# Optimization experiments

Hardware: AMD Instinct MI355X
Metric: run time of the kernel (lower is better)

Reference implementation:

```python
import jax, jax.numpy as jnp
from jax import lax
import numpy as np

B, CTX, TGT, D_MODEL = 2, 1024, 256, 512
EXPAND, D_STATE, D_CONV, N_LAYERS = 2, 16, 4, 2
D_INNER = EXPAND * D_MODEL
DT_RANK = (D_MODEL + 15) // 16  # 32, mamba_ssm default ceil(d_model/16)
LN_EPS = 1e-5


def setup_inputs() -> dict:
    key = jax.random.key(0)
    ks = jax.random.split(key, 20)
    s = 0.02
    inp = {
        "context_repr": jax.random.normal(ks[0], (B, CTX, D_MODEL), jnp.float32),
        "target_time_emb": jax.random.normal(ks[1], (B, TGT, D_MODEL), jnp.float32),
        "target_var_emb": jax.random.normal(ks[2], (B, TGT, D_MODEL), jnp.float32),
        "target_count": TGT,
        # position_proj / output_proj / LayerNorm params
        "pos_w": jax.random.normal(ks[3], (D_MODEL, 2 * D_MODEL), jnp.float32) * s,
        "pos_b": jnp.zeros((D_MODEL,), jnp.float32),
        "outp_w": jax.random.normal(ks[4], (D_MODEL, D_MODEL), jnp.float32) * s,
        "outp_b": jnp.zeros((D_MODEL,), jnp.float32),
        "ln_g": jnp.ones((D_MODEL,), jnp.float32),
        "ln_b": jnp.zeros((D_MODEL,), jnp.float32),
        # stacked per-layer Mamba params
        "in_w": jax.random.normal(ks[5], (N_LAYERS, 2 * D_INNER, D_MODEL), jnp.float32) * s,
        "conv_w": jax.random.normal(ks[6], (N_LAYERS, D_INNER, D_CONV), jnp.float32) * s,
        "conv_b": jnp.zeros((N_LAYERS, D_INNER), jnp.float32),
        "xproj_w": jax.random.normal(ks[7], (N_LAYERS, DT_RANK + 2 * D_STATE, D_INNER), jnp.float32) * s,
        "dt_w": jax.random.normal(ks[8], (N_LAYERS, D_INNER, DT_RANK), jnp.float32) * s,
        "dt_b": jax.random.normal(ks[9], (N_LAYERS, D_INNER), jnp.float32) * s,
        # A_log init as in mamba_ssm: A = arange(1, d_state+1) repeated over d_inner
        "A_log": jnp.broadcast_to(
            jnp.log(jnp.arange(1, D_STATE + 1, dtype=jnp.float32)),
            (N_LAYERS, D_INNER, D_STATE),
        ).copy(),
        "D_skip": jnp.ones((N_LAYERS, D_INNER), jnp.float32),
        "out_w": jax.random.normal(ks[10], (N_LAYERS, D_MODEL, D_INNER), jnp.float32) * s,
    }
    return inp


def _mamba_block(x, in_w, conv_w, conv_b, xproj_w, dt_w, dt_b, A_log, D_skip, out_w):
    # x: [B, L, d_model]
    Bb, L, _ = x.shape
    xz = jnp.einsum("bld,ed->ble", x, in_w)          # [B, L, 2*d_inner]
    xc, z = jnp.split(xz, 2, axis=-1)
    # causal depthwise conv1d (Conv1d pad=d_conv-1 then [..., :L])
    xt = xc.transpose(0, 2, 1)                        # [B, d_inner, L]
    conv = lax.conv_general_dilated(
        xt, conv_w[:, None, :], (1,), [(D_CONV - 1, 0)],
        feature_group_count=D_INNER,
        dimension_numbers=("NCH", "OIH", "NCH"),
    )
    u = jax.nn.silu(conv + conv_b[None, :, None]).transpose(0, 2, 1)  # [B, L, d_inner]
    x_dbl = jnp.einsum("bld,ed->ble", u, xproj_w)     # [B, L, dt_rank + 2*d_state]
    dt, Bm, Cm = jnp.split(x_dbl, [DT_RANK, DT_RANK + D_STATE], axis=-1)
    delta = jax.nn.softplus(jnp.einsum("blr,dr->bld", dt, dt_w) + dt_b)  # [B, L, d_inner]
    A = -jnp.exp(A_log)                               # [d_inner, d_state]
    dA = jnp.exp(delta[..., None] * A)                # [B, L, d_inner, d_state]
    dBu = delta[..., None] * Bm[:, :, None, :] * u[..., None]

    def step(h, inps):
        dA_t, dBu_t, C_t = inps                       # [B,d_inner,d_state], same, [B,d_state]
        h = dA_t * h + dBu_t
        y = jnp.einsum("bds,bs->bd", h, C_t)
        return h, y

    h0 = jnp.zeros((Bb, D_INNER, D_STATE), x.dtype)
    _, ys = lax.scan(step, h0, (dA.transpose(1, 0, 2, 3), dBu.transpose(1, 0, 2, 3), Cm.transpose(1, 0, 2)))
    y = ys.transpose(1, 0, 2) + u * D_skip            # [B, L, d_inner]
    y = y * jax.nn.silu(z)
    return jnp.einsum("ble,de->bld", y, out_w)        # [B, L, d_model]


def reference(context_repr, target_time_emb, target_var_emb, target_count,
              pos_w, pos_b, outp_w, outp_b, ln_g, ln_b,
              in_w, conv_w, conv_b, xproj_w, dt_w, dt_b, A_log, D_skip, out_w):
    tc = jnp.concatenate([target_time_emb, target_var_emb], axis=-1)      # [B, T, 2*d]
    pos = jnp.einsum("blk,dk->bld", tc, pos_w) + pos_b                    # [B, T, d]
    x = jnp.concatenate([context_repr, pos], axis=1)                      # [B, C+T, d]
    for i in range(N_LAYERS):
        x = x + _mamba_block(x, in_w[i], conv_w[i], conv_b[i], xproj_w[i],
                             dt_w[i], dt_b[i], A_log[i], D_skip[i], out_w[i])
    mu = jnp.mean(x, axis=-1, keepdims=True)
    var = jnp.mean(jnp.square(x - mu), axis=-1, keepdims=True)
    x = (x - mu) * lax.rsqrt(var + LN_EPS) * ln_g + ln_b
    tgt = x[:, -int(target_count):]
    return jnp.einsum("bld,ed->ble", tgt, outp_w) + outp_b
```

## Files before the change

### kernel.cpp

```cpp
#include <hip/hip_runtime.h>
#include <hip/hip_bf16.h>

#define B_     2
#define CTX_   1024
#define TGT_   256
#define DM_    512
#define L_     1280
#define DI_    1024
#define DS_    16
#define DCONV_ 4
#define NL_    2
#define DTR_   32
#define MROWS_ (B_*L_)
#define NC_    80
#define CL_    16
#define XDBL_N_ (MROWS_*64)

typedef unsigned short u16;
typedef __attribute__((ext_vector_type(8))) __bf16 bf16x8;
typedef __attribute__((ext_vector_type(4))) float f32x4;

__device__ __forceinline__ float sigmoidf_(float v){ return 1.f/(1.f+__expf(-v)); }
__device__ __forceinline__ float siluf_(float v){ return v*sigmoidf_(v); }
__device__ __forceinline__ float softplusf_(float v){ return (v>20.f)?v:log1pf(__expf(v)); }
__device__ __forceinline__ u16 f2b(float f){
    union { float f; unsigned u; } x; x.f = f;
    unsigned u = x.u;
    return (u16)((u + 0x7fffu + ((u>>16)&1u)) >> 16);
}
__device__ __forceinline__ float b2f(u16 v){ return __uint_as_float(((unsigned)v)<<16); }
__device__ __forceinline__ void gload_lds16(const void* g, void* l){
    __builtin_amdgcn_global_load_lds((const __attribute__((address_space(1))) unsigned*)g,
                                     (__attribute__((address_space(3))) unsigned*)l, 16, 0, 0);
}

#define G0_ 262144
#define G1_ 131072
#define G2_  65536
#define G3_  32768
#define G4_  16384
__global__ __launch_bounds__(256) void k_f2b_all(const float* __restrict__ s0, const float* __restrict__ s1,
                                                 const float* __restrict__ s2, const float* __restrict__ s3,
                                                 const float* __restrict__ s4,
                                                 u16* d0, u16* d1, u16* d2, u16* d3, u16* d4){
    int g = blockIdx.x*256 + threadIdx.x;
    const float* s; u16* d; int base;
    if      (g < G0_)                { s=s0; d=d0; base=g*8; }
    else if (g < G0_+G1_)            { s=s1; d=d1; base=(g-G0_)*8; }
    else if (g < G0_+G1_+G2_)        { s=s2; d=d2; base=(g-G0_-G1_)*8; }
    else if (g < G0_+G1_+G2_+G3_)    { s=s3; d=d3; base=(g-G0_-G1_-G2_)*8; }
    else                             { s=s4; d=d4; base=(g-G0_-G1_-G2_-G3_)*8; }
    float4 a = *(const float4*)&s[base];
    float4 b = *(const float4*)&s[base+4];
    union { u16 us[8]; uint4 v; } o;
    o.us[0]=f2b(a.x); o.us[1]=f2b(a.y); o.us[2]=f2b(a.z); o.us[3]=f2b(a.w);
    o.us[4]=f2b(b.x); o.us[5]=f2b(b.y); o.us[6]=f2b(b.z); o.us[7]=f2b(b.w);
    *(uint4*)&d[base] = o.v;
}

__global__ __launch_bounds__(256) void k_pre(const float* __restrict__ ctx, const float* __restrict__ te,
                                             const float* __restrict__ ve, float* __restrict__ x,
                                             u16* __restrict__ xb, u16* __restrict__ tcb){
    int blk = blockIdx.x;
    if (blk < 1024){
        int e = (blk*256 + threadIdx.x)*4;
        int d = e % DM_;
        int l = (e/DM_) % CTX_;
        int b = e/(DM_*CTX_);
        float4 v = *(const float4*)&ctx[e];
        size_t o = ((size_t)(b*L_+l))*DM_ + d;
        *(float4*)&x[o] = v;
        union { u16 us[4]; uint2 q; } p;
        p.us[0]=f2b(v.x); p.us[1]=f2b(v.y); p.us[2]=f2b(v.z); p.us[3]=f2b(v.w);
        *(uint2*)&xb[o] = p.q;
    } else {
        int e = ((blk-1024)*256 + threadIdx.x)*4;
        int k = e % (2*DM_);
        int r = e / (2*DM_);
        float4 v = (k < DM_) ? *(const float4*)&te[(size_t)r*DM_ + k]
                             : *(const float4*)&ve[(size_t)r*DM_ + (k-DM_)];
        union { u16 us[4]; uint2 q; } p;
        p.us[0]=f2b(v.x); p.us[1]=f2b(v.y); p.us[2]=f2b(v.z); p.us[3]=f2b(v.w);
        *(uint2*)&tcb[e] = p.q;
    }
}

__global__ __launch_bounds__(256) void k_conv_silu(const u16* __restrict__ xzb, const float* __restrict__ cw,
                                                   const float* __restrict__ cb, u16* __restrict__ ub){
    int e = (blockIdx.x*256 + threadIdx.x)*4;
    int d = e % DI_;
    int l = (e/DI_) % L_;
    int b = e/(DI_*L_);
    const u16* base = xzb + (size_t)b*L_*2048 + d;
    float4 w0 = *(const float4*)&cw[(d+0)*4];
    float4 w1 = *(const float4*)&cw[(d+1)*4];
    float4 w2 = *(const float4*)&cw[(d+2)*4];
    float4 w3 = *(const float4*)&cw[(d+3)*4];
    float4 bb = *(const float4*)&cb[d];
    float a0=bb.x, a1=bb.y, a2=bb.z, a3=bb.w;
    #pragma unroll
    for (int k=0;k<DCONV_;++k){
        int ll = l-3+k;
        if (ll >= 0){
            uint2 q = *(const uint2*)&base[(size_t)ll*2048];
            float x0=b2f((u16)(q.x&0xffffu)), x1=b2f((u16)(q.x>>16));
            float x2=b2f((u16)(q.y&0xffffu)), x3=b2f((u16)(q.y>>16));
            float c0 = (k==0)?w0.x:(k==1)?w0.y:(k==2)?w0.z:w0.w;
            float c1 = (k==0)?w1.x:(k==1)?w1.y:(k==2)?w1.z:w1.w;
            float c2 = (k==0)?w2.x:(k==1)?w2.y:(k==2)?w2.z:w2.w;
            float c3 = (k==0)?w3.x:(k==1)?w3.y:(k==2)?w3.z:w3.w;
            a0=fmaf(x0,c0,a0); a1=fmaf(x1,c1,a1); a2=fmaf(x2,c2,a2); a3=fmaf(x3,c3,a3);
        }
    }
    union { u16 us[4]; uint2 q; } o;
    o.us[0]=f2b(siluf_(a0)); o.us[1]=f2b(siluf_(a1));
    o.us[2]=f2b(siluf_(a2)); o.us[3]=f2b(siluf_(a3));
    *(uint2*)&ub[e] = o.q;
}

template<bool WB>
__global__ __launch_bounds__(256) void k_mmx(const u16* __restrict__ A, int lda,
                                             const u16* __restrict__ Bw, int ldb,
                                             float* __restrict__ C, int ldc,
                                             const float* __restrict__ bias, int K,
                                             u16* __restrict__ Cb, int ldcb){
    __shared__ u16 As[128*32];
    __shared__ u16 Bs[128*32];
    int tid = threadIdx.x;
    int wave = tid >> 6, lane = tid & 63;
    int bm = blockIdx.y*128, bn = blockIdx.x*128;
    int wr = (wave>>1)*64, wc = (wave&1)*64;
    f32x4 acc[4][4] = {};
    int lrow = lane & 15, lk = (lane>>4)*8;
    int dphys0 = wave*1024 + lane*16;
    int dphys1 = dphys0 + 4096;
    int alog0  = dphys0 ^ (((dphys0>>7)&7)<<4);
    int alog1  = dphys1 ^ (((dphys1>>7)&7)<<4);
    int grow0  = alog0 >> 6,        grow1  = alog1 >> 6;
    int gcol0  = (alog0 & 63) >> 1, gcol1  = (alog1 & 63) >> 1;
    u16* AsW0 = &As[wave*512];         u16* AsW1 = &As[2048 + wave*512];
    u16* BsW0 = &Bs[wave*512];         u16* BsW1 = &Bs[2048 + wave*512];
    int aoff[4], boff[4];
    #pragma unroll
    for (int f=0; f<4; ++f){
        int ra = wr + f*16 + lrow, rb = wc + f*16 + lrow;
        aoff[f] = (ra*64 + lk*2) ^ (((ra>>1)&7)<<4);
        boff[f] = (rb*64 + lk*2) ^ (((rb>>1)&7)<<4);
    }
    for (int k0 = 0; k0 < K; k0 += 32){
        gload_lds16(&A [(size_t)(bm+grow0)*lda + k0 + gcol0], AsW0);
        gload_lds16(&A [(size_t)(bm+grow1)*lda + k0 + gcol1], AsW1);
        gload_lds16(&Bw[(size_t)(bn+grow0)*ldb + k0 + gcol0], BsW0);
        gload_lds16(&Bw[(size_t)(bn+grow1)*ldb + k0 + gcol1], BsW1);
        __syncthreads();
        bf16x8 af[4], bfr[4];
        #pragma unroll
        for (int f=0; f<4; ++f){
            af [f] = *(const bf16x8*)((const char*)As + aoff[f]);
            bfr[f] = *(const bf16x8*)((const char*)Bs + boff[f]);
        }
        #pragma unroll
        for (int fm=0; fm<4; ++fm)
            #pragma unroll
            for (int fn=0; fn<4; ++fn)
                acc[fm][fn] = __builtin_amdgcn_mfma_f32_16x16x32_bf16(af[fm], bfr[fn], acc[fm][fn], 0,0,0);
        __syncthreads();
    }
    #pragma unroll
    for (int fm=0; fm<4; ++fm){
        int m0 = bm + wr + fm*16 + (lane>>4)*4;
        #pragma unroll
        for (int fn=0; fn<4; ++fn){
            int n = bn + wc + fn*16 + (lane&15);
            float bsv = (!WB && bias) ? bias[n] : 0.f;
            #pragma unroll
            for (int j=0; j<4; ++j){
                float v = acc[fm][fn][j] + bsv;
                if (WB) Cb[(size_t)(m0+j)*ldcb + n] = f2b(v);
                else    C [(size_t)(m0+j)*ldc  + n] = v;
            }
        }
    }
}

template<bool ACC, bool SPLIT, bool SCAT>
__global__ __launch_bounds__(256) void k_mmx64(const u16* __restrict__ A, int lda,
                                               const u16* __restrict__ Bw, int ldb,
                                               float* __restrict__ C, int ldc,
                                               const float* __restrict__ bias, int ksteps,
                                               u16* __restrict__ Cb, int ldcb, int splitStride){
    __shared__ u16 As[64*32];
    __shared__ u16 Bs[64*32];
    int tid = threadIdx.x;
    int wave = tid >> 6, lane = tid & 63;
    int bm = blockIdx.y*64;
    int bn    = SPLIT ? 0 : blockIdx.x*64;
    int kbase = SPLIT ? blockIdx.x*ksteps*32 : 0;
    int wr = (wave>>1)*32, wc = (wave&1)*32;
    f32x4 acc[2][2] = {};
    int lrow = lane & 15, lk = (lane>>4)*8;
    int dphys = wave*1024 + lane*16;
    int alog  = dphys ^ (((dphys>>7)&7)<<4);
    int grow  = alog >> 6;
    int gcol  = (alog & 63) >> 1;
    u16* AsW = &As[wave*512];
    u16* BsW = &Bs[wave*512];
    int aoff[2], boff[2];
    #pragma unroll
    for (int f=0; f<2; ++f){
        int ra = wr + f*16 + lrow, rb = wc + f*16 + lrow;
        aoff[f] = (ra*64 + lk*2) ^ (((ra>>1)&7)<<4);
        boff[f] = (rb*64 + lk*2) ^ (((rb>>1)&7)<<4);
    }
    for (int s = 0; s < ksteps; ++s){
        int k0 = kbase + s*32;
        gload_lds16(&A [(size_t)(bm+grow)*lda + k0 + gcol], AsW);
        gload_lds16(&Bw[(size_t)(bn+grow)*ldb + k0 + gcol], BsW);
        __syncthreads();
        bf16x8 af[2], bfr[2];
        #pragma unroll
        for (int f=0; f<2; ++f){
            af [f] = *(const bf16x8*)((const char*)As + aoff[f]);
            bfr[f] = *(const bf16x8*)((const char*)Bs + boff[f]);
        }
        #pragma unroll
        for (int fm=0; fm<2; ++fm)
            #pragma unroll
            for (int fn=0; fn<2; ++fn)
                acc[fm][fn] = __builtin_amdgcn_mfma_f32_16x16x32_bf16(af[fm], bfr[fn], acc[fm][fn], 0,0,0);
        __syncthreads();
    }
    float* Cout = SPLIT ? (C + (size_t)blockIdx.x*splitStride) : C;
    #pragma unroll
    for (int fm=0; fm<2; ++fm){
        int m0 = bm + wr + fm*16 + (lane>>4)*4;
        #pragma unroll
        for (int fn=0; fn<2; ++fn){
            int n = bn + wc + fn*16 + (lane&15);
            float bsv = (!SPLIT && bias) ? bias[n] : 0.f;
            #pragma unroll
            for (int j=0; j<4; ++j){
                float v = acc[fm][fn][j] + bsv;
                int m = m0 + j;
                if (SCAT){
                    int xrow = (m>>8)*L_ + CTX_ + (m&255);
                    C [(size_t)xrow*ldc  + n] = v;
                    Cb[(size_t)xrow*ldcb + n] = f2b(v);
                } else {
                    size_t off = (size_t)m*ldc + n;
                    if (ACC) v += Cout[off];
                    Cout[off] = v;
                    if (!SPLIT && Cb) Cb[(size_t)m*ldcb + n] = f2b(v);
                }
            }
        }
    }
}

__global__ __launch_bounds__(256) void k_red8(const float* __restrict__ part, float* __restrict__ out){
    int j = (blockIdx.x*256 + threadIdx.x)*4;
    float4 s = *(const float4*)&part[j];
    #pragma unroll
    for (int p=1;p<8;++p){
        float4 t = *(const float4*)&part[(size_t)p*XDBL_N_ + j];
        s.x+=t.x; s.y+=t.y; s.z+=t.z; s.w+=t.w;
    }
    *(float4*)&out[j] = s;
}

__global__ __launch_bounds__(256) void k_scan1(const u16* __restrict__ ub, const float* __restrict__ xdbl,
                                               const float* __restrict__ dtw, const float* __restrict__ dtb,
                                               const float* __restrict__ Alog,
                                               float* __restrict__ hend, float* __restrict__ P){
    __shared__ float sX[CL_*64];
    __shared__ float sW[64*33];
    __shared__ float sDtb[64];
    __shared__ float sDel[CL_*64];
    __shared__ u16   sU[CL_*64];
    int blk = blockIdx.x;
    int dgrp = blk & 15;
    int c = (blk>>4) % NC_;
    int b = blk/(16*NC_);
    int d0 = dgrp*64;
    int tid = threadIdx.x;
    size_t rowbase = (size_t)(b*L_ + c*CL_);
    {
        int e = tid*4;
        *(float4*)&sX[e] = *(const float4*)&xdbl[rowbase*64 + e];
        int st=e>>6, dd=e&63;
        *(uint2*)&sU[e] = *(const uint2*)&ub[(rowbase+st)*DI_ + d0 + dd];
        int w0 = tid*8, dr = w0>>5, kk = w0&31;
        float4 wa = *(const float4*)&dtw[(size_t)(d0+dr)*DTR_ + kk];
        float4 wb = *(const float4*)&dtw[(size_t)(d0+dr)*DTR_ + kk + 4];
        sW[dr*33+kk+0]=wa.x; sW[dr*33+kk+1]=wa.y; sW[dr*33+kk+2]=wa.z; sW[dr*33+kk+3]=wa.w;
        sW[dr*33+kk+4]=wb.x; sW[dr*33+kk+5]=wb.y; sW[dr*33+kk+6]=wb.z; sW[dr*33+kk+7]=wb.w;
        if (tid < 64) sDtb[tid] = dtb[d0+tid];
    }
    __syncthreads();
    #pragma unroll
    for (int i=0;i<4;++i){
        int idx = tid + i*256;
        int t = idx>>6, dd = idx&63;
        float acc = sDtb[dd];
        #pragma unroll
        for (int k=0;k<DTR_;++k) acc = fmaf(sX[t*64+k], sW[dd*33+k], acc);
        sDel[idx] = softplusf_(acc);
    }
    __syncthreads();
    int dl = tid>>2, sg = (tid&3)*4;
    int d = d0 + dl;
    float A[4];
    #pragma unroll
    for (int i=0;i<4;++i) A[i] = -__expf(Alog[d*DS_ + sg + i]);
    float h[4] = {0,0,0,0}, Pl[4] = {1.f,1.f,1.f,1.f};
    #pragma unroll
    for (int t=0;t<CL_;++t){
        float delta = sDel[t*64+dl];
        float uu    = b2f(sU[t*64+dl]);
        float du    = delta*uu;
        #pragma unroll
        for (int i=0;i<4;++i){
            float a = __expf(delta*A[i]);
            h[i]  = fmaf(a, h[i], du*sX[t*64 + 32 + sg + i]);
            Pl[i] *= a;
        }
    }
    size_t ob = ((size_t)((b*NC_+c)*DI_) + d)*DS_ + sg;
    *(float4*)&hend[ob] = make_float4(h[0],h[1],h[2],h[3]);
    *(float4*)&P[ob]    = make_float4(Pl[0],Pl[1],Pl[2],Pl[3]);
}

__global__ __launch_bounds__(256) void k_scan2(float* __restrict__ hend, const float* __restrict__ P){
    int g = blockIdx.x*256 + threadIdx.x;
    int s = g & 15;
    int d = (g>>4) & 1023;
    int b = g>>14;
    size_t base = ((size_t)b*NC_*DI_ + d)*DS_ + s;
    const size_t cs = (size_t)DI_*DS_;
    float h = 0.f;
    for (int c0=0;c0<NC_;c0+=8){
        float he[8], p[8];
        #pragma unroll
        for (int j=0;j<8;++j){ size_t idx = base + (size_t)(c0+j)*cs; he[j]=hend[idx]; p[j]=P[idx]; }
        #pragma unroll
        for (int j=0;j<8;++j){ size_t idx = base + (size_t)(c0+j)*cs; hend[idx]=h; h=fmaf(p[j],h,he[j]); }
    }
}

__global__ __launch_bounds__(256) void k_scan3(const u16* __restrict__ ub, const float* __restrict__ xdbl,
                                               const float* __restrict__ dtw, const float* __restrict__ dtb,
                                               const u16* __restrict__ xzb,
                                               const float* __restrict__ Alog, const float* __restrict__ Dsk,
                                               const float* __restrict__ hstart, u16* __restrict__ yb){
    __shared__ float sX[CL_*64];
    __shared__ float sW[64*33];
    __shared__ float sDtb[64];
    __shared__ float sDel[CL_*64];
    __shared__ u16   sU[CL_*64];
    __shared__ float sY[CL_*64];
    int blk = blockIdx.x;
    int dgrp = blk & 15;
    int c = (blk>>4) % NC_;
    int b = blk/(16*NC_);
    int d0 = dgrp*64;
    int tid = threadIdx.x;
    size_t rowbase = (size_t)(b*L_ + c*CL_);
    {
        int e = tid*4;
        *(float4*)&sX[e] = *(const float4*)&xdbl[rowbase*64 + e];
        int st=e>>6, dd=e&63;
        *(uint2*)&sU[e] = *(const uint2*)&ub[(rowbase+st)*DI_ + d0 + dd];
        int w0 = tid*8, dr = w0>>5, kk = w0&31;
        float4 wa = *(const float4*)&dtw[(size_t)(d0+dr)*DTR_ + kk];
        float4 wb = *(const float4*)&dtw[(size_t)(d0+dr)*DTR_ + kk + 4];
        sW[dr*33+kk+0]=wa.x; sW[dr*33+kk+1]=wa.y; sW[dr*33+kk+2]=wa.z; sW[dr*33+kk+3]=wa.w;
        sW[dr*33+kk+4]=wb.x; sW[dr*33+kk+5]=wb.y; sW[dr*33+kk+6]=wb.z; sW[dr*33+kk+7]=wb.w;
        if (tid < 64) sDtb[tid] = dtb[d0+tid];
    }
    __syncthreads();
    #pragma unroll
    for (int i=0;i<4;++i){
        int idx = tid + i*256;
        int t = idx>>6, dd = idx&63;
        float acc = sDtb[dd];
        #pragma unroll
        for (int k=0;k<DTR_;++k) acc = fmaf(sX[t*64+k], sW[dd*33+k], acc);
        sDel[idx] = softplusf_(acc);
    }
    __syncthreads();
    int dl = tid>>2, sg = (tid&3)*4;
    int d = d0 + dl;
    float A[4];
    #pragma unroll
    for (int i=0;i<4;++i) A[i] = -__expf(Alog[d*DS_ + sg + i]);
    size_t ib = ((size_t)((b*NC_+c)*DI_) + d)*DS_ + sg;
    float4 h4 = *(const float4*)&hstart[ib];
    float h[4] = {h4.x, h4.y, h4.z, h4.w};
    #pragma unroll
    for (int t=0;t<CL_;++t){
        float delta = sDel[t*64+dl];
        float uu    = b2f(sU[t*64+dl]);
        float du    = delta*uu;
        float yt = 0.f;
        #pragma unroll
        for (int i=0;i<4;++i){
            float a = __expf(delta*A[i]);
            h[i] = fmaf(a, h[i], du*sX[t*64 + 32 + sg + i]);
            yt   = fmaf(h[i], sX[t*64 + 48 + sg + i], yt);
        }
        yt += __shfl_xor(yt, 1);
        yt += __shfl_xor(yt, 2);
        if ((tid&3)==0) sY[t*64+dl] = yt;
    }
    __syncthreads();
    {
        int e = tid*4, st = e>>6, dd = e&63;
        size_t off = (rowbase+st)*DI_ + d0 + dd;
        float4 dskv = *(const float4*)&Dsk[d0+dd];
        uint2 zz = *(const uint2*)&xzb[(rowbase+st)*2048 + DI_ + d0 + dd];
        float z0 = __uint_as_float(zz.x<<16),  z1 = __uint_as_float(zz.x & 0xffff0000u);
        float z2 = __uint_as_float(zz.y<<16),  z3 = __uint_as_float(zz.y & 0xffff0000u);
        float u0 = b2f(sU[e+0]), u1 = b2f(sU[e+1]), u2 = b2f(sU[e+2]), u3 = b2f(sU[e+3]);
        union { u16 us[4]; uint2 q; } o;
        o.us[0] = f2b((sY[e+0] + u0*dskv.x) * siluf_(z0));
        o.us[1] = f2b((sY[e+1] + u1*dskv.y) * siluf_(z1));
        o.us[2] = f2b((sY[e+2] + u2*dskv.z) * siluf_(z2));
        o.us[3] = f2b((sY[e+3] + u3*dskv.w) * siluf_(z3));
        *(uint2*)&yb[off] = o.q;
    }
}

__global__ __launch_bounds__(256) void k_ln_tgt(const float* __restrict__ x, const float* __restrict__ g_,
                                                const float* __restrict__ b_, u16* __restrict__ xnb){
    int r = blockIdx.x;
    int b = r / TGT_, t = r % TGT_;
    const float* row = x + ((size_t)(b*L_+CTX_+t))*DM_;
    int tid = threadIdx.x;
    float2 v = *(const float2*)&row[tid*2];
    float s = v.x+v.y, sq = v.x*v.x+v.y*v.y;
    #pragma unroll
    for (int off=32; off; off>>=1){ s += __shfl_down(s,off); sq += __shfl_down(sq,off); }
    __shared__ float ss[4], ssq[4];
    int w = tid>>6, ln = tid&63;
    if (ln==0){ ss[w]=s; ssq[w]=sq; }
    __syncthreads();
    if (tid==0){
        float S=ss[0]+ss[1]+ss[2]+ss[3], Q=ssq[0]+ssq[1]+ssq[2]+ssq[3];
        float mu = S/(float)DM_;
        float var = Q/(float)DM_ - mu*mu;
        ss[0]=mu; ssq[0]=rsqrtf(var+1e-5f);
    }
    __syncthreads();
    float mu=ss[0], rs=ssq[0];
    xnb[(size_t)r*DM_ + tid*2+0] = f2b((v.x-mu)*rs*g_[tid*2+0] + b_[tid*2+0]);
    xnb[(size_t)r*DM_ + tid*2+1] = f2b((v.y-mu)*rs*g_[tid*2+1] + b_[tid*2+1]);
}

extern "C" void kernel_launch(void* const* d_in, const int* in_sizes, int n_in,
                              void* d_out, int out_size, void* d_ws, size_t ws_size,
                              hipStream_t stream) {
    const float* ctx    = (const float*)d_in[0];
    const float* te     = (const float*)d_in[1];
    const float* ve     = (const float*)d_in[2];
    const float* pos_w  = (const float*)d_in[4];
    const float* pos_b  = (const float*)d_in[5];
    const float* outp_w = (const float*)d_in[6];
    const float* outp_b = (const float*)d_in[7];
    const float* ln_g   = (const float*)d_in[8];
    const float* ln_b   = (const float*)d_in[9];
    const float* in_w   = (const float*)d_in[10];
    const float* conv_w = (const float*)d_in[11];
    const float* conv_b = (const float*)d_in[12];
    const float* xproj_w= (const float*)d_in[13];
    const float* dt_w   = (const float*)d_in[14];
    const float* dt_b   = (const float*)d_in[15];
    const float* A_log  = (const float*)d_in[16];
    const float* D_skip = (const float*)d_in[17];
    const float* out_w  = (const float*)d_in[18];
    float* out = (float*)d_out;

    float* ws    = (float*)d_ws;
    float* x     = ws;
    float* xdbl  = x     + 1310720;
    float* hend  = xdbl  + 163840;
    float* P     = hend  + 2621440;
    float* xdblp = P     + 2621440;
    u16*  xb    = (u16*)(xdblp + 1310720);
    u16*  tcb   = xb    + 1310720;
    u16*  yb    = tcb   + 524288;
    u16*  xnb   = yb    + 2621440;
    u16*  ub    = xnb   + 262144;
    u16*  xzb   = ub    + 2621440;
    u16*  inwb  = xzb   + 5242880;
    u16*  outwb = inwb  + 2097152;
    u16*  poswb = outwb + 1048576;
    u16*  outpwb= poswb + 524288;
    u16*  xpwb  = outpwb+ 262144;

    k_f2b_all<<<1984, 256, 0, stream>>>(in_w, out_w, pos_w, outp_w, xproj_w,
                                        inwb, outwb, poswb, outpwb, xpwb);
    k_pre<<<1536, 256, 0, stream>>>(ctx, te, ve, x, xb, tcb);
    k_mmx64<false,false,true><<<dim3(8,8), 256, 0, stream>>>(tcb, 2*DM_, poswb, 2*DM_, x, DM_, pos_b, 32, xb, DM_, 0);

    for (int i=0;i<NL_;++i){
        const u16*   inwbi  = inwb + (size_t)i*2*DI_*DM_;
        const float* cw     = conv_w  + (size_t)i*DI_*DCONV_;
        const float* cb     = conv_b  + (size_t)i*DI_;
        const u16*   xpwbi  = xpwb + (size_t)i*(DTR_+2*DS_)*DI_;
        const float* dtw    = dt_w    + (size_t)i*DI_*DTR_;
        const float* dtb    = dt_b    + (size_t)i*DI_;
        const float* Ai     = A_log   + (size_t)i*DI_*DS_;
        const float* Dsk    = D_skip  + (size_t)i*DI_;
        const u16*   outwbi = outwb + (size_t)i*DM_*DI_;

        k_mmx<true><<<dim3(16,20), 256, 0, stream>>>(xb, DM_, inwbi, DM_, nullptr, 0, nullptr, DM_, xzb, 2*DI_);
        k_conv_silu<<<2560, 256, 0, stream>>>(xzb, cw, cb, ub);
        k_mmx64<false,true,false><<<dim3(8,40), 256, 0, stream>>>(ub, DI_, xpwbi, DI_, xdblp, 64, nullptr, 4, nullptr, 0, XDBL_N_);
        k_red8<<<160, 256, 0, stream>>>(xdblp, xdbl);
        k_scan1<<<2560, 256, 0, stream>>>(ub, xdbl, dtw, dtb, Ai, hend, P);
        k_scan2<<<128, 256, 0, stream>>>(hend, P);
        k_scan3<<<2560, 256, 0, stream>>>(ub, xdbl, dtw, dtb, xzb, Ai, Dsk, hend, yb);
        k_mmx64<true,false,false><<<dim3(8,40), 256, 0, stream>>>(yb, DI_, outwbi, DI_, x, DM_, nullptr, 32, xb, DM_, 0);
    }

    k_ln_tgt<<<512, 256, 0, stream>>>(x, ln_g, ln_b, xnb);
    k_mmx64<false,false,false><<<dim3(8,8), 256, 0, stream>>>(xnb, DM_, outpwb, DM_, out, DM_, outp_b, 16, nullptr, 0, 0);
}
```

Baseline: 250.6 us.

## Double-buffer GEMM LDS tiles, merge init kernels, use longer scan chunks

Both bf16 GEMM kernels now use two LDS buffers, so the global-to-LDS loads for the next K tile are issued before the MFMAs on the current tile, with one explicit vmcnt wait and barrier per step. The two setup kernels (weight conversion and input packing) are merged into a single launch to save one launch gap. The chunked scan now uses 40 chunks of 32 steps instead of 80 of 16, which halves the scan block count, the sequential cross-chunk pass and the hend/P workspace, at the cost of a longer serial loop inside each block. Double buffering doubles LDS use per block and may lower occupancy.

```diff
diff --git a/kernel.cpp b/kernel.cpp
--- a/kernel.cpp
+++ b/kernel.cpp
@@ -12,8 +12,8 @@
 #define NL_    2
 #define DTR_   32
 #define MROWS_ (B_*L_)
-#define NC_    80
-#define CL_    16
+#define NC_    40
+#define CL_    32
 #define XDBL_N_ (MROWS_*64)
 
 typedef unsigned short u16;
@@ -33,37 +33,40 @@
     __builtin_amdgcn_global_load_lds((const __attribute__((address_space(1))) unsigned*)g,
                                      (__attribute__((address_space(3))) unsigned*)l, 16, 0, 0);
 }
+#define PIPE_SYNC do{ asm volatile("s_waitcnt vmcnt(0)" ::: "memory"); \
+                      __builtin_amdgcn_sched_barrier(0); \
+                      __builtin_amdgcn_s_barrier(); \
+                      __builtin_amdgcn_sched_barrier(0); }while(0)
 
 #define G0_ 262144
 #define G1_ 131072
 #define G2_  65536
 #define G3_  32768
 #define G4_  16384
-__global__ __launch_bounds__(256) void k_f2b_all(const float* __restrict__ s0, const float* __restrict__ s1,
-                                                 const float* __restrict__ s2, const float* __restrict__ s3,
-                                                 const float* __restrict__ s4,
-                                                 u16* d0, u16* d1, u16* d2, u16* d3, u16* d4){
-    int g = blockIdx.x*256 + threadIdx.x;
-    const float* s; u16* d; int base;
-    if      (g < G0_)                { s=s0; d=d0; base=g*8; }
-    else if (g < G0_+G1_)            { s=s1; d=d1; base=(g-G0_)*8; }
-    else if (g < G0_+G1_+G2_)        { s=s2; d=d2; base=(g-G0_-G1_)*8; }
-    else if (g < G0_+G1_+G2_+G3_)    { s=s3; d=d3; base=(g-G0_-G1_-G2_)*8; }
-    else                             { s=s4; d=d4; base=(g-G0_-G1_-G2_-G3_)*8; }
-    float4 a = *(const float4*)&s[base];
-    float4 b = *(const float4*)&s[base+4];
-    union { u16 us[8]; uint4 v; } o;
-    o.us[0]=f2b(a.x); o.us[1]=f2b(a.y); o.us[2]=f2b(a.z); o.us[3]=f2b(a.w);
-    o.us[4]=f2b(b.x); o.us[5]=f2b(b.y); o.us[6]=f2b(b.z); o.us[7]=f2b(b.w);
-    *(uint4*)&d[base] = o.v;
-}
-
-__global__ __launch_bounds__(256) void k_pre(const float* __restrict__ ctx, const float* __restrict__ te,
-                                             const float* __restrict__ ve, float* __restrict__ x,
-                                             u16* __restrict__ xb, u16* __restrict__ tcb){
+__global__ __launch_bounds__(256) void k_init(const float* __restrict__ s0, const float* __restrict__ s1,
+                                              const float* __restrict__ s2, const float* __restrict__ s3,
+                                              const float* __restrict__ s4,
+                                              u16* d0, u16* d1, u16* d2, u16* d3, u16* d4,
+                                              const float* __restrict__ ctx, const float* __restrict__ te,
+                                              const float* __restrict__ ve, float* __restrict__ x,
+                                              u16* __restrict__ xb, u16* __restrict__ tcb){
     int blk = blockIdx.x;
-    if (blk < 1024){
-        int e = (blk*256 + threadIdx.x)*4;
+    if (blk < 1984){
+        int g = blk*256 + threadIdx.x;
+        const float* s; u16* d; int base;
+        if      (g < G0_)                { s=s0; d=d0; base=g*8; }
+        else if (g < G0_+G1_)            { s=s1; d=d1; base=(g-G0_)*8; }
+        else if (g < G0_+G1_+G2_)        { s=s2; d=d2; base=(g-G0_-G1_)*8; }
+        else if (g < G0_+G1_+G2_+G3_)    { s=s3; d=d3; base=(g-G0_-G1_-G2_)*8; }
+        else                             { s=s4; d=d4; base=(g-G0_-G1_-G2_-G3_)*8; }
+        float4 a = *(const float4*)&s[base];
+        float4 b = *(const float4*)&s[base+4];
+        union { u16 us[8]; uint4 v; } o;
+        o.us[0]=f2b(a.x); o.us[1]=f2b(a.y); o.us[2]=f2b(a.z); o.us[3]=f2b(a.w);
+        o.us[4]=f2b(b.x); o.us[5]=f2b(b.y); o.us[6]=f2b(b.z); o.us[7]=f2b(b.w);
+        *(uint4*)&d[base] = o.v;
+    } else if (blk < 1984+1024){
+        int e = ((blk-1984)*256 + threadIdx.x)*4;
         int d = e % DM_;
         int l = (e/DM_) % CTX_;
         int b = e/(DM_*CTX_);
@@ -74,7 +77,7 @@
         p.us[0]=f2b(v.x); p.us[1]=f2b(v.y); p.us[2]=f2b(v.z); p.us[3]=f2b(v.w);
         *(uint2*)&xb[o] = p.q;
     } else {
-        int e = ((blk-1024)*256 + threadIdx.x)*4;
+        int e = ((blk-1984-1024)*256 + threadIdx.x)*4;
         int k = e % (2*DM_);
         int r = e / (2*DM_);
         float4 v = (k < DM_) ? *(const float4*)&te[(size_t)r*DM_ + k]
@@ -124,8 +127,8 @@
                                              float* __restrict__ C, int ldc,
                                              const float* __restrict__ bias, int K,
                                              u16* __restrict__ Cb, int ldcb){
-    __shared__ u16 As[128*32];
-    __shared__ u16 Bs[128*32];
+    __shared__ u16 As[2][128*32];
+    __shared__ u16 Bs[2][128*32];
     int tid = threadIdx.x;
     int wave = tid >> 6, lane = tid & 63;
     int bm = blockIdx.y*128, bn = blockIdx.x*128;
@@ -138,8 +141,10 @@
     int alog1  = dphys1 ^ (((dphys1>>7)&7)<<4);
     int grow0  = alog0 >> 6,        grow1  = alog1 >> 6;
     int gcol0  = (alog0 & 63) >> 1, gcol1  = (alog1 & 63) >> 1;
-    u16* AsW0 = &As[wave*512];         u16* AsW1 = &As[2048 + wave*512];
-    u16* BsW0 = &Bs[wave*512];         u16* BsW1 = &Bs[2048 + wave*512];
+    const u16* Ar0 = A  + (size_t)(bm+grow0)*lda + gcol0;
+    const u16* Ar1 = A  + (size_t)(bm+grow1)*lda + gcol1;
+    const u16* Br0 = Bw + (size_t)(bn+grow0)*ldb + gcol0;
+    const u16* Br1 = Bw + (size_t)(bn+grow1)*ldb + gcol1;
     int aoff[4], boff[4];
     #pragma unroll
     for (int f=0; f<4; ++f){
@@ -147,24 +152,32 @@
         aoff[f] = (ra*64 + lk*2) ^ (((ra>>1)&7)<<4);
         boff[f] = (rb*64 + lk*2) ^ (((rb>>1)&7)<<4);
     }
-    for (int k0 = 0; k0 < K; k0 += 32){
-        gload_lds16(&A [(size_t)(bm+grow0)*lda + k0 + gcol0], AsW0);
-        gload_lds16(&A [(size_t)(bm+grow1)*lda + k0 + gcol1], AsW1);
-        gload_lds16(&Bw[(size_t)(bn+grow0)*ldb + k0 + gcol0], BsW0);
-        gload_lds16(&Bw[(size_t)(bn+grow1)*ldb + k0 + gcol1], BsW1);
-        __syncthreads();
+    int nt = K >> 5;
+    auto stage = [&](int t, int buf){
+        int k0 = t*32;
+        gload_lds16(Ar0 + k0, &As[buf][wave*512]);
+        gload_lds16(Ar1 + k0, &As[buf][2048 + wave*512]);
+        gload_lds16(Br0 + k0, &Bs[buf][wave*512]);
+        gload_lds16(Br1 + k0, &Bs[buf][2048 + wave*512]);
+    };
+    stage(0, 0);
+    PIPE_SYNC;
+    int cur = 0;
+    for (int t=0; t<nt; ++t){
+        if (t+1 < nt) stage(t+1, cur^1);
         bf16x8 af[4], bfr[4];
         #pragma unroll
         for (int f=0; f<4; ++f){
-            af [f] = *(const bf16x8*)((const char*)As + aoff[f]);
-            bfr[f] = *(const bf16x8*)((const char*)Bs + boff[f]);
+            af [f] = *(const bf16x8*)((const char*)As[cur] + aoff[f]);
+            bfr[f] = *(const bf16x8*)((const char*)Bs[cur] + boff[f]);
         }
         #pragma unroll
         for (int fm=0; fm<4; ++fm)
             #pragma unroll
             for (int fn=0; fn<4; ++fn)
                 acc[fm][fn] = __builtin_amdgcn_mfma_f32_16x16x32_bf16(af[fm], bfr[fn], acc[fm][fn], 0,0,0);
-        __syncthreads();
+        PIPE_SYNC;
+        cur ^= 1;
     }
     #pragma unroll
     for (int fm=0; fm<4; ++fm){
@@ -189,8 +202,8 @@
                                                float* __restrict__ C, int ldc,
                                                const float* __restrict__ bias, int ksteps,
                                                u16* __restrict__ Cb, int ldcb, int splitStride){
-    __shared__ u16 As[64*32];
-    __shared__ u16 Bs[64*32];
+    __shared__ u16 As[2][64*32];
+    __shared__ u16 Bs[2][64*32];
     int tid = threadIdx.x;
     int wave = tid >> 6, lane = tid & 63;
     int bm = blockIdx.y*64;
@@ -203,8 +216,8 @@
     int alog  = dphys ^ (((dphys>>7)&7)<<4);
     int grow  = alog >> 6;
     int gcol  = (alog & 63) >> 1;
-    u16* AsW = &As[wave*512];
-    u16* BsW = &Bs[wave*512];
+    const u16* Ar = A  + (size_t)(bm+grow)*lda + gcol;
+    const u16* Br = Bw + (size_t)(bn+grow)*ldb + gcol;
     int aoff[2], boff[2];
     #pragma unroll
     for (int f=0; f<2; ++f){
@@ -212,23 +225,29 @@
         aoff[f] = (ra*64 + lk*2) ^ (((ra>>1)&7)<<4);
         boff[f] = (rb*64 + lk*2) ^ (((rb>>1)&7)<<4);
     }
-    for (int s = 0; s < ksteps; ++s){
-        int k0 = kbase + s*32;
-        gload_lds16(&A [(size_t)(bm+grow)*lda + k0 + gcol], AsW);
-        gload_lds16(&Bw[(size_t)(bn+grow)*ldb + k0 + gcol], BsW);
-        __syncthreads();
+    auto stage = [&](int t, int buf){
+        int k0 = kbase + t*32;
+        gload_lds16(Ar + k0, &As[buf][wave*512]);
+        gload_lds16(Br + k0, &Bs[buf][wave*512]);
+    };
+    stage(0, 0);
+    PIPE_SYNC;
+    int cur = 0;
+    for (int t = 0; t < ksteps; ++t){
+        if (t+1 < ksteps) stage(t+1, cur^1);
         bf16x8 af[2], bfr[2];
         #pragma unroll
         for (int f=0; f<2; ++f){
-            af [f] = *(const bf16x8*)((const char*)As + aoff[f]);
-            bfr[f] = *(const bf16x8*)((const char*)Bs + boff[f]);
+            af [f] = *(const bf16x8*)((const char*)As[cur] + aoff[f]);
+            bfr[f] = *(const bf16x8*)((const char*)Bs[cur] + boff[f]);
         }
         #pragma unroll
         for (int fm=0; fm<2; ++fm)
             #pragma unroll
             for (int fn=0; fn<2; ++fn)
                 acc[fm][fn] = __builtin_amdgcn_mfma_f32_16x16x32_bf16(af[fm], bfr[fn], acc[fm][fn], 0,0,0);
-        __syncthreads();
+        PIPE_SYNC;
+        cur ^= 1;
     }
     float* Cout = SPLIT ? (C + (size_t)blockIdx.x*splitStride) : C;
     #pragma unroll
@@ -284,11 +303,14 @@
     int d0 = dgrp*64;
     int tid = threadIdx.x;
     size_t rowbase = (size_t)(b*L_ + c*CL_);
-    {
-        int e = tid*4;
+    #pragma unroll
+    for (int j=0;j<2;++j){
+        int e = tid*4 + j*1024;
         *(float4*)&sX[e] = *(const float4*)&xdbl[rowbase*64 + e];
         int st=e>>6, dd=e&63;
         *(uint2*)&sU[e] = *(const uint2*)&ub[(rowbase+st)*DI_ + d0 + dd];
+    }
+    {
         int w0 = tid*8, dr = w0>>5, kk = w0&31;
         float4 wa = *(const float4*)&dtw[(size_t)(d0+dr)*DTR_ + kk];
         float4 wb = *(const float4*)&dtw[(size_t)(d0+dr)*DTR_ + kk + 4];
@@ -298,7 +320,7 @@
     }
     __syncthreads();
     #pragma unroll
-    for (int i=0;i<4;++i){
+    for (int i=0;i<8;++i){
         int idx = tid + i*256;
         int t = idx>>6, dd = idx&63;
         float acc = sDtb[dd];
@@ -365,11 +387,14 @@
     int d0 = dgrp*64;
     int tid = threadIdx.x;
     size_t rowbase = (size_t)(b*L_ + c*CL_);
-    {
-        int e = tid*4;
+    #pragma unroll
+    for (int j=0;j<2;++j){
+        int e = tid*4 + j*1024;
         *(float4*)&sX[e] = *(const float4*)&xdbl[rowbase*64 + e];
         int st=e>>6, dd=e&63;
         *(uint2*)&sU[e] = *(const uint2*)&ub[(rowbase+st)*DI_ + d0 + dd];
+    }
+    {
         int w0 = tid*8, dr = w0>>5, kk = w0&31;
         float4 wa = *(const float4*)&dtw[(size_t)(d0+dr)*DTR_ + kk];
         float4 wb = *(const float4*)&dtw[(size_t)(d0+dr)*DTR_ + kk + 4];
@@ -379,7 +404,7 @@
     }
     __syncthreads();
     #pragma unroll
-    for (int i=0;i<4;++i){
+    for (int i=0;i<8;++i){
         int idx = tid + i*256;
         int t = idx>>6, dd = idx&63;
         float acc = sDtb[dd];
@@ -413,8 +438,9 @@
         if ((tid&3)==0) sY[t*64+dl] = yt;
     }
     __syncthreads();
-    {
-        int e = tid*4, st = e>>6, dd = e&63;
+    #pragma unroll
+    for (int j=0;j<2;++j){
+        int e = tid*4 + j*1024, st = e>>6, dd = e&63;
         size_t off = (rowbase+st)*DI_ + d0 + dd;
         float4 dskv = *(const float4*)&Dsk[d0+dd];
         uint2 zz = *(const uint2*)&xzb[(rowbase+st)*2048 + DI_ + d0 + dd];
@@ -483,8 +509,8 @@
     float* x     = ws;
     float* xdbl  = x     + 1310720;
     float* hend  = xdbl  + 163840;
-    float* P     = hend  + 2621440;
-    float* xdblp = P     + 2621440;
+    float* P     = hend  + 1310720;
+    float* xdblp = P     + 1310720;
     u16*  xb    = (u16*)(xdblp + 1310720);
     u16*  tcb   = xb    + 1310720;
     u16*  yb    = tcb   + 524288;
@@ -497,9 +523,9 @@
     u16*  outpwb= poswb + 524288;
     u16*  xpwb  = outpwb+ 262144;
 
-    k_f2b_all<<<1984, 256, 0, stream>>>(in_w, out_w, pos_w, outp_w, xproj_w,
-                                        inwb, outwb, poswb, outpwb, xpwb);
-    k_pre<<<1536, 256, 0, stream>>>(ctx, te, ve, x, xb, tcb);
+    k_init<<<3520, 256, 0, stream>>>(in_w, out_w, pos_w, outp_w, xproj_w,
+                                     inwb, outwb, poswb, outpwb, xpwb,
+                                     ctx, te, ve, x, xb, tcb);
     k_mmx64<false,false,true><<<dim3(8,8), 256, 0, stream>>>(tcb, 2*DM_, poswb, 2*DM_, x, DM_, pos_b, 32, xb, DM_, 0);
 
     for (int i=0;i<NL_;++i){
@@ -517,9 +543,9 @@
         k_conv_silu<<<2560, 256, 0, stream>>>(xzb, cw, cb, ub);
         k_mmx64<false,true,false><<<dim3(8,40), 256, 0, stream>>>(ub, DI_, xpwbi, DI_, xdblp, 64, nullptr, 4, nullptr, 0, XDBL_N_);
         k_red8<<<160, 256, 0, stream>>>(xdblp, xdbl);
-        k_scan1<<<2560, 256, 0, stream>>>(ub, xdbl, dtw, dtb, Ai, hend, P);
+        k_scan1<<<1280, 256, 0, stream>>>(ub, xdbl, dtw, dtb, Ai, hend, P);
         k_scan2<<<128, 256, 0, stream>>>(hend, P);
-        k_scan3<<<2560, 256, 0, stream>>>(ub, xdbl, dtw, dtb, xzb, Ai, Dsk, hend, yb);
+        k_scan3<<<1280, 256, 0, stream>>>(ub, xdbl, dtw, dtb, xzb, Ai, Dsk, hend, yb);
         k_mmx64<true,false,false><<<dim3(8,40), 256, 0, stream>>>(yb, DI_, outwbi, DI_, x, DM_, nullptr, 32, xb, DM_, 0);
     }
 
```

Result: no change. 250.2 us (-0.2%).
